# Performance work log

Hardware: AMD Instinct MI355X
Metric: run time of the kernel (lower is better)

## Reference

```python
import jax, jax.numpy as jnp
import numpy as np

THETA = 10000.0


def rope_apply(x, pos, theta=THETA):
    # x: [..., S, d] with d even; rotates interleaved pairs (2k, 2k+1),
    # matching the block-diag 2x2 rotation matmul in the torch RoPE.
    d = x.shape[-1]
    half = d // 2
    inv_freq = 1.0 / (theta ** (2.0 * jnp.arange(half, dtype=jnp.float32) / d))
    ang = pos.astype(jnp.float32)[:, None] * inv_freq[None, :]  # [S, half]
    cos, sin = jnp.cos(ang), jnp.sin(ang)
    xe, xo = x[..., 0::2], x[..., 1::2]
    oe = cos * xe - sin * xo
    oo = sin * xe + cos * xo
    return jnp.stack([oe, oo], axis=-1).reshape(x.shape)


def setup_inputs() -> dict:
    key = jax.random.key(0)
    ks = jax.random.split(key, 5)
    B, S, D = 2, 2048, 1024
    scale = 0.02
    return {
        "x": jax.random.normal(ks[0], (B, S, D), dtype=jnp.float32),
        "token_positions": jnp.arange(S, dtype=jnp.int64 if jax.config.jax_enable_x64 else jnp.int32),
        "wq": jax.random.normal(ks[1], (D, D), dtype=jnp.float32) * scale,
        "wk": jax.random.normal(ks[2], (D, D), dtype=jnp.float32) * scale,
        "wv": jax.random.normal(ks[3], (D, D), dtype=jnp.float32) * scale,
        "wo": jax.random.normal(ks[4], (D, D), dtype=jnp.float32) * scale,
    }


def reference(x, token_positions, wq, wk, wv, wo):
    B, S, D = x.shape
    H = 16
    dk = D // H

    def split_heads(t):  # [B,S,D] -> [B,H,S,dk]
        return t.reshape(B, S, H, dk).swapaxes(1, 2)

    q = split_heads(jnp.einsum('bsd,ed->bse', x, wq))
    k = split_heads(jnp.einsum('bsd,ed->bse', x, wk))
    v = split_heads(jnp.einsum('bsd,ed->bse', x, wv))

    q = rope_apply(q, token_positions)
    k = rope_apply(k, token_positions)

    scores = jnp.einsum('bhqd,bhkd->bhqk', q, k) / jnp.sqrt(jnp.float32(dk))
    causal = jnp.tril(jnp.ones((S, S), dtype=bool))
    scores = jnp.where(causal, scores, -jnp.inf)
    p = jax.nn.softmax(scores, axis=-1)
    o = jnp.einsum('bhqk,bhkd->bhqd', p, v)          # [B,H,S,dk]
    o = o.swapaxes(1, 2).reshape(B, S, D)            # merge heads
    return jnp.einsum('bse,de->bsd', o, wo)          # out proj (wo.T)
```

## Files before the change

kernel.cpp:

```cpp
#include <hip/hip_runtime.h>

typedef unsigned short u16;
typedef __attribute__((ext_vector_type(8))) short short8;
typedef __attribute__((ext_vector_type(4))) float f32x4;

__device__ __forceinline__ u16 f2b(float f) {
  union { float f; unsigned u; } v; v.f = f;
  unsigned u = v.u;
  return (u16)((u + 0x7FFFu + ((u >> 16) & 1u)) >> 16);
}
__device__ __forceinline__ u16 f2b_trunc(float f) {
  union { float f; unsigned u; } v; v.f = f;
  return (u16)(v.u >> 16);
}
__device__ __forceinline__ void glds16(const u16* g, u16* l) {
  __builtin_amdgcn_global_load_lds((const __attribute__((address_space(1))) void*)g,
                                   (__attribute__((address_space(3))) void*)l, 16, 0, 0);
}

__global__ __launch_bounds__(256) void prep_k(const float* __restrict__ x,
                                              const float* __restrict__ wq,
                                              const float* __restrict__ wk,
                                              const float* __restrict__ wv,
                                              const float* __restrict__ wo,
                                              const int* __restrict__ pos,
                                              u16* __restrict__ xb,
                                              u16* __restrict__ wqkvb,
                                              u16* __restrict__ wob,
                                              float* __restrict__ ct,
                                              float* __restrict__ st) {
  int bx = blockIdx.x, tid = threadIdx.x;
  if (bx < 8192) {
    const float* src; u16* dst; int base;
    if (bx < 4096)      { src = x;  dst = xb;                base = bx; }
    else if (bx < 5120) { src = wq; dst = wqkvb;             base = bx - 4096; }
    else if (bx < 6144) { src = wk; dst = wqkvb + (1 << 20); base = bx - 5120; }
    else if (bx < 7168) { src = wv; dst = wqkvb + (2 << 20); base = bx - 6144; }
    else                { src = wo; dst = wob;               base = bx - 7168; }
    int i4 = base * 1024 + tid * 4;
    const float4 v = *(const float4*)(src + i4);
    uint2 o;
    o.x = (unsigned)f2b(v.x) | ((unsigned)f2b(v.y) << 16);
    o.y = (unsigned)f2b(v.z) | ((unsigned)f2b(v.w) << 16);
    *(uint2*)(dst + i4) = o;
  } else {
    int idx = (bx - 8192) * 256 + tid;
    int i = idx & 31, s = idx >> 5;
    float p = (float)pos[s];
    float inv = expf(-(float)i * (logf(10000.0f) / 32.0f));
    float ang = p * inv;
    ct[idx] = cosf(ang);
    st[idx] = sinf(ang);
  }
}

__global__ __launch_bounds__(256) void gemm_qkv(const u16* __restrict__ A,
                                                const u16* __restrict__ B,
                                                const float* __restrict__ ct,
                                                const float* __restrict__ st,
                                                u16* __restrict__ Qr,
                                                u16* __restrict__ Kr,
                                                u16* __restrict__ VTg) {
  const int M = 4096, N = 3072, K = 1024;
  (void)M; (void)N;
  __shared__ u16 As[128 * 32];
  __shared__ u16 Bs[128 * 32];
  const int tid = threadIdx.x;
  const int wv = tid >> 6, lane = tid & 63;
  const int quad = lane >> 4, l16 = lane & 15;
  const int wm = wv & 1, wn = wv >> 1;
  const int m0 = blockIdx.y * 128, n0 = blockIdx.x * 128;

  f32x4 acc[4][4];
  for (int i = 0; i < 4; i++)
    for (int j = 0; j < 4; j++) acc[i][j] = (f32x4){0.f, 0.f, 0.f, 0.f};

  for (int kt = 0; kt < K; kt += 32) {
    __syncthreads();
#pragma unroll
    for (int pass = 0; pass < 2; pass++) {
      int c = pass * 256 + tid;
      int row = c >> 2, k8 = c & 3;
      glds16(A + (size_t)(m0 + row) * K + kt + k8 * 8, As + (size_t)(c & ~63) * 8);
      glds16(B + (size_t)(n0 + row) * K + kt + k8 * 8, Bs + (size_t)(c & ~63) * 8);
    }
    __syncthreads();
    short8 af[4], bfr[4];
#pragma unroll
    for (int i = 0; i < 4; i++)
      af[i] = *(const short8*)(As + (wm * 64 + i * 16 + l16) * 32 + quad * 8);
#pragma unroll
    for (int j = 0; j < 4; j++)
      bfr[j] = *(const short8*)(Bs + (wn * 64 + j * 16 + l16) * 32 + quad * 8);
#pragma unroll
    for (int i = 0; i < 4; i++)
#pragma unroll
      for (int j = 0; j < 4; j++)
        acc[i][j] = __builtin_amdgcn_mfma_f32_16x16x32_bf16(af[i], bfr[j], acc[i][j], 0, 0, 0);
  }

  const int region = n0 >> 10;
  if (region < 2) {
    u16* dst = region ? Kr : Qr;
    const int par = l16 & 1;
    for (int i = 0; i < 4; i++)
      for (int j = 0; j < 4; j++) {
        int col = n0 + wn * 64 + j * 16 + l16;
        int cq = col & 1023;
        int h = cq >> 6, d = cq & 63, ifr = (d >> 1) & 31;
        for (int r = 0; r < 4; r++) {
          int row = m0 + wm * 64 + i * 16 + quad * 4 + r;
          int b = row >> 11, s = row & 2047;
          float v = acc[i][j][r];
          float vp = __shfl_xor(v, 1);
          float c = ct[s * 32 + ifr], sn = st[s * 32 + ifr];
          float o = par ? (sn * vp + c * v) : (c * v - sn * vp);
          dst[((size_t)(b * 16 + h) * 2048 + s) * 64 + d] = f2b(o);
        }
      }
  } else {
    for (int i = 0; i < 4; i++)
      for (int j = 0; j < 4; j++) {
        int col = n0 + wn * 64 + j * 16 + l16;
        int cq = col & 1023;
        int h = cq >> 6, d = cq & 63;
        for (int r = 0; r < 4; r++) {
          int row = m0 + wm * 64 + i * 16 + quad * 4 + r;
          int b = row >> 11, s = row & 2047;
          VTg[((size_t)(b * 16 + h) * 64 + d) * 2048 + s] = f2b(acc[i][j][r]);
        }
      }
  }
}

__global__ __launch_bounds__(256) void gemm_bt_f32(const u16* __restrict__ A,
                                                   const u16* __restrict__ B,
                                                   float* __restrict__ C,
                                                   int M, int N, int K) {
  __shared__ u16 As[128 * 32];
  __shared__ u16 Bs[128 * 32];
  const int tid = threadIdx.x;
  const int wv = tid >> 6, lane = tid & 63;
  const int quad = lane >> 4, l16 = lane & 15;
  const int wm = wv & 1, wn = wv >> 1;
  const int m0 = blockIdx.y * 128, n0 = blockIdx.x * 128;

  f32x4 acc[4][4];
  for (int i = 0; i < 4; i++)
    for (int j = 0; j < 4; j++) acc[i][j] = (f32x4){0.f, 0.f, 0.f, 0.f};

  for (int kt = 0; kt < K; kt += 32) {
    __syncthreads();
#pragma unroll
    for (int pass = 0; pass < 2; pass++) {
      int c = pass * 256 + tid;
      int row = c >> 2, k8 = c & 3;
      glds16(A + (size_t)(m0 + row) * K + kt + k8 * 8, As + (size_t)(c & ~63) * 8);
      glds16(B + (size_t)(n0 + row) * K + kt + k8 * 8, Bs + (size_t)(c & ~63) * 8);
    }
    __syncthreads();
    short8 af[4], bfr[4];
#pragma unroll
    for (int i = 0; i < 4; i++)
      af[i] = *(const short8*)(As + (wm * 64 + i * 16 + l16) * 32 + quad * 8);
#pragma unroll
    for (int j = 0; j < 4; j++)
      bfr[j] = *(const short8*)(Bs + (wn * 64 + j * 16 + l16) * 32 + quad * 8);
#pragma unroll
    for (int i = 0; i < 4; i++)
#pragma unroll
      for (int j = 0; j < 4; j++)
        acc[i][j] = __builtin_amdgcn_mfma_f32_16x16x32_bf16(af[i], bfr[j], acc[i][j], 0, 0, 0);
  }
  for (int i = 0; i < 4; i++)
    for (int j = 0; j < 4; j++) {
      int col = n0 + wn * 64 + j * 16 + l16;
      for (int r = 0; r < 4; r++) {
        int row = m0 + wm * 64 + i * 16 + quad * 4 + r;
        C[(size_t)row * N + col] = acc[i][j][r];
      }
    }
}

__global__ __launch_bounds__(256) void attn_k(const u16* __restrict__ Q,
                                              const u16* __restrict__ K,
                                              const u16* __restrict__ VT,
                                              float* __restrict__ Op,
                                              float* __restrict__ Lp, int S) {
  __shared__ u16 Qs[8 * 512], Ks[8 * 512], Vt[64 * 64], Ps[8 * 520];
  const int tid = threadIdx.x;
  const int wv = tid >> 6, lane = tid & 63, quad = lane >> 4, l16 = lane & 15;
  const int bh = blockIdx.y, par = blockIdx.z;
  const u16* Qg = Q + (size_t)bh * S * 64;
  const u16* Kg = K + (size_t)bh * S * 64;
  const u16* Vg = VT + (size_t)bh * S * 64;
  const int nqt = S >> 6;
  const float scale2 = 0.125f * 1.44269504f;
  const int rowbase = wv * 16 + quad * 4;
  float* Opb = Op + ((size_t)par * 32 + bh) * S * 64;
  float* Lpb = Lp + ((size_t)par * 32 + bh) * S;

  const int vrow_off = lane >> 3;
  const int vchunk = (lane & 7) ^ (lane >> 3);

  for (int t = 0; t < 2; t++) {
    const int qt = t ? (nqt - 1 - (int)blockIdx.x) : (int)blockIdx.x;
    const int q0 = qt * 64;
    for (int p = wv; p < 8; p += 4)
      glds16(Qg + (size_t)(q0 + lane) * 64 + p * 8, Qs + p * 512);
    __syncthreads();
    short8 qa0 = *(const short8*)(Qs + quad * 512 + (wv * 16 + l16) * 8);
    short8 qa1 = *(const short8*)(Qs + (4 + quad) * 512 + (wv * 16 + l16) * 8);

    f32x4 oacc[4];
    for (int j = 0; j < 4; j++) oacc[j] = (f32x4){0.f, 0.f, 0.f, 0.f};
    float l_r[4] = {0.f, 0.f, 0.f, 0.f};

    for (int kt = par; kt <= qt; kt += 2) {
      const int k0 = kt * 64;
      __syncthreads();
      for (int p = wv; p < 8; p += 4) {
        glds16(Kg + (size_t)(k0 + lane) * 64 + p * 8, Ks + p * 512);
        glds16(Vg + (size_t)(p * 8 + vrow_off) * S + k0 + vchunk * 8, Vt + p * 512);
      }
      __syncthreads();

      const bool diag = (kt == qt);
#pragma unroll
      for (int nt = 0; nt < 4; nt++) {
        f32x4 s4 = (f32x4){0.f, 0.f, 0.f, 0.f};
        short8 b0 = *(const short8*)(Ks + quad * 512 + (nt * 16 + l16) * 8);
        short8 b1 = *(const short8*)(Ks + (4 + quad) * 512 + (nt * 16 + l16) * 8);
        s4 = __builtin_amdgcn_mfma_f32_16x16x32_bf16(qa0, b0, s4, 0, 0, 0);
        s4 = __builtin_amdgcn_mfma_f32_16x16x32_bf16(qa1, b1, s4, 0, 0, 0);
        int col = nt * 16 + l16;
        int cp = col >> 3, co = col & 7;
#pragma unroll
        for (int r = 0; r < 4; r++) {
          float v = s4[r] * scale2;
          v = fminf(v, 86.f);
          if (diag && col > rowbase + r) v = -1e30f;
          float p = exp2f(v);
          l_r[r] += p;
          int row = rowbase + r;
          int A = (cp + 2 * (row >> 3)) & 7;
          Ps[A * 520 + row * 8 + co] = f2b_trunc(p);
        }
      }
      {
        int mr = wv * 16 + l16;
        int A0 = (quad + 2 * (mr >> 3)) & 7;
        short8 pa0 = *(const short8*)(Ps + A0 * 520 + mr * 8);
        short8 pa1 = *(const short8*)(Ps + ((A0 + 4) & 7) * 520 + mr * 8);
        int sl0 = quad ^ (l16 & 7);
#pragma unroll
        for (int nt = 0; nt < 4; nt++) {
          int d = nt * 16 + l16;
          short8 vb0 = *(const short8*)(Vt + d * 64 + sl0 * 8);
          short8 vb1 = *(const short8*)(Vt + d * 64 + (sl0 ^ 4) * 8);
          oacc[nt] = __builtin_amdgcn_mfma_f32_16x16x32_bf16(pa0, vb0, oacc[nt], 0, 0, 0);
          oacc[nt] = __builtin_amdgcn_mfma_f32_16x16x32_bf16(pa1, vb1, oacc[nt], 0, 0, 0);
        }
      }
    }
#pragma unroll
    for (int r = 0; r < 4; r++) {
      l_r[r] += __shfl_xor(l_r[r], 1);
      l_r[r] += __shfl_xor(l_r[r], 2);
      l_r[r] += __shfl_xor(l_r[r], 4);
      l_r[r] += __shfl_xor(l_r[r], 8);
    }
    if (l16 == 0)
#pragma unroll
      for (int r = 0; r < 4; r++) Lpb[q0 + rowbase + r] = l_r[r];
#pragma unroll
    for (int nt = 0; nt < 4; nt++) {
      int col = nt * 16 + l16;
#pragma unroll
      for (int r = 0; r < 4; r++)
        Opb[(size_t)(q0 + rowbase + r) * 64 + col] = oacc[nt][r];
    }
    __syncthreads();
  }
}

__global__ __launch_bounds__(256) void combine_k(const float* __restrict__ Op,
                                                 const float* __restrict__ Lp,
                                                 u16* __restrict__ O, int S) {
  int idx = blockIdx.x * 256 + threadIdx.x;
  int d4 = idx & 15, s = (idx >> 4) & 2047, bh = idx >> 15;
  size_t po = (((size_t)bh * S) + s) * 64 + d4 * 4;
  size_t pstride = (size_t)32 * S * 64;
  float4 a = *(const float4*)(Op + po);
  float4 c = *(const float4*)(Op + pstride + po);
  float l = Lp[(size_t)bh * S + s] + Lp[(size_t)32 * S + (size_t)bh * S + s];
  float rl = 1.f / l;
  int b = bh >> 4, h = bh & 15;
  size_t oo = ((size_t)(b * S + s) * 16 + h) * 64 + d4 * 4;
  uint2 o;
  o.x = (unsigned)f2b((a.x + c.x) * rl) | ((unsigned)f2b((a.y + c.y) * rl) << 16);
  o.y = (unsigned)f2b((a.z + c.z) * rl) | ((unsigned)f2b((a.w + c.w) * rl) << 16);
  *(uint2*)(O + oo) = o;
}

extern "C" void kernel_launch(void* const* d_in, const int* in_sizes, int n_in,
                              void* d_out, int out_size, void* d_ws, size_t ws_size,
                              hipStream_t stream) {
  const float* x  = (const float*)d_in[0];
  const int*   tp = (const int*)d_in[1];
  const float* wq = (const float*)d_in[2];
  const float* wk = (const float*)d_in[3];
  const float* wvp = (const float*)d_in[4];
  const float* wo = (const float*)d_in[5];
  float* out = (float*)d_out;

  const int B = 2, S = 2048, D = 1024;
  const int BS = B * S;
  (void)B; (void)D;

  char* ws = (char*)d_ws;
  u16*   xb    = (u16*)(ws);
  u16*   wqkvb = (u16*)(ws + ((size_t)8 << 20));
  u16*   wob   = (u16*)(ws + ((size_t)14 << 20));
  float* ct    = (float*)(ws + ((size_t)16 << 20));
  float* st    = (float*)(ws + ((size_t)16 << 20) + (256 << 10));
  u16*   qr    = (u16*)(ws + ((size_t)17 << 20));
  u16*   kr    = (u16*)(ws + ((size_t)25 << 20));
  u16*   vtg   = (u16*)(ws + ((size_t)33 << 20));
  float* lpart = (float*)(ws + ((size_t)41 << 20));
  u16*   ob    = (u16*)(ws + ((size_t)42 << 20));
  float* opart = (float*)(ws + ((size_t)50 << 20));

  prep_k<<<8448, 256, 0, stream>>>(x, wq, wk, wvp, wo, tp, xb, wqkvb, wob, ct, st);

  dim3 g1(3 * D / 128, BS / 128);
  gemm_qkv<<<g1, 256, 0, stream>>>(xb, wqkvb, ct, st, qr, kr, vtg);

  dim3 ga(S / 128, 32, 2);
  attn_k<<<ga, 256, 0, stream>>>(qr, kr, vtg, opart, lpart, S);

  combine_k<<<(32 * S * 16) / 256, 256, 0, stream>>>(opart, lpart, ob, S);

  dim3 g2(D / 128, BS / 128);
  gemm_bt_f32<<<g2, 256, 0, stream>>>(ob, wob, out, BS, D, D);
}
```

Before: 216.2 us.

## Swizzle GEMM LDS tiles and vectorize QKV epilogue stores

```diff
diff --git a/kernel.cpp b/kernel.cpp
--- a/kernel.cpp
+++ b/kernel.cpp
@@ -27,8 +27,7 @@
                                               u16* __restrict__ xb,
                                               u16* __restrict__ wqkvb,
                                               u16* __restrict__ wob,
-                                              float* __restrict__ ct,
-                                              float* __restrict__ st) {
+                                              float* __restrict__ cs) {
   int bx = blockIdx.x, tid = threadIdx.x;
   if (bx < 8192) {
     const float* src; u16* dst; int base;
@@ -49,20 +48,18 @@
     float p = (float)pos[s];
     float inv = expf(-(float)i * (logf(10000.0f) / 32.0f));
     float ang = p * inv;
-    ct[idx] = cosf(ang);
-    st[idx] = sinf(ang);
+    cs[idx * 2]     = cosf(ang);
+    cs[idx * 2 + 1] = sinf(ang);
   }
 }
 
 __global__ __launch_bounds__(256) void gemm_qkv(const u16* __restrict__ A,
                                                 const u16* __restrict__ B,
-                                                const float* __restrict__ ct,
-                                                const float* __restrict__ st,
+                                                const float* __restrict__ cs,
                                                 u16* __restrict__ Qr,
                                                 u16* __restrict__ Kr,
                                                 u16* __restrict__ VTg) {
-  const int M = 4096, N = 3072, K = 1024;
-  (void)M; (void)N;
+  const int K = 1024;
   __shared__ u16 As[128 * 32];
   __shared__ u16 Bs[128 * 32];
   const int tid = threadIdx.x;
@@ -70,6 +67,7 @@
   const int quad = lane >> 4, l16 = lane & 15;
   const int wm = wv & 1, wn = wv >> 1;
   const int m0 = blockIdx.y * 128, n0 = blockIdx.x * 128;
+  const int kk = (quad ^ ((l16 >> 1) & 3)) * 8;
 
   f32x4 acc[4][4];
   for (int i = 0; i < 4; i++)
@@ -80,7 +78,7 @@
 #pragma unroll
     for (int pass = 0; pass < 2; pass++) {
       int c = pass * 256 + tid;
-      int row = c >> 2, k8 = c & 3;
+      int row = c >> 2, k8 = (c & 3) ^ ((row >> 1) & 3);
       glds16(A + (size_t)(m0 + row) * K + kt + k8 * 8, As + (size_t)(c & ~63) * 8);
       glds16(B + (size_t)(n0 + row) * K + kt + k8 * 8, Bs + (size_t)(c & ~63) * 8);
     }
@@ -88,10 +86,10 @@
     short8 af[4], bfr[4];
 #pragma unroll
     for (int i = 0; i < 4; i++)
-      af[i] = *(const short8*)(As + (wm * 64 + i * 16 + l16) * 32 + quad * 8);
+      af[i] = *(const short8*)(As + (wm * 64 + i * 16 + l16) * 32 + kk);
 #pragma unroll
     for (int j = 0; j < 4; j++)
-      bfr[j] = *(const short8*)(Bs + (wn * 64 + j * 16 + l16) * 32 + quad * 8);
+      bfr[j] = *(const short8*)(Bs + (wn * 64 + j * 16 + l16) * 32 + kk);
 #pragma unroll
     for (int i = 0; i < 4; i++)
 #pragma unroll
@@ -100,36 +98,42 @@
   }
 
   const int region = n0 >> 10;
+  const int b = m0 >> 11;
   if (region < 2) {
     u16* dst = region ? Kr : Qr;
-    const int par = l16 & 1;
+    const bool evn = (l16 & 1) == 0;
     for (int i = 0; i < 4; i++)
       for (int j = 0; j < 4; j++) {
         int col = n0 + wn * 64 + j * 16 + l16;
         int cq = col & 1023;
         int h = cq >> 6, d = cq & 63, ifr = (d >> 1) & 31;
         for (int r = 0; r < 4; r++) {
-          int row = m0 + wm * 64 + i * 16 + quad * 4 + r;
-          int b = row >> 11, s = row & 2047;
+          int s = (m0 & 2047) + wm * 64 + i * 16 + quad * 4 + r;
           float v = acc[i][j][r];
           float vp = __shfl_xor(v, 1);
-          float c = ct[s * 32 + ifr], sn = st[s * 32 + ifr];
-          float o = par ? (sn * vp + c * v) : (c * v - sn * vp);
-          dst[((size_t)(b * 16 + h) * 2048 + s) * 64 + d] = f2b(o);
+          if (evn) {
+            float2 c2 = *(const float2*)(cs + (s * 32 + ifr) * 2);
+            float oe = c2.x * v - c2.y * vp;
+            float oo = c2.y * v + c2.x * vp;
+            unsigned pk = (unsigned)f2b(oe) | ((unsigned)f2b(oo) << 16);
+            *(unsigned*)(dst + ((size_t)(b * 16 + h) * 2048 + s) * 64 + d) = pk;
+          }
         }
       }
   } else {
-    for (int i = 0; i < 4; i++)
-      for (int j = 0; j < 4; j++) {
-        int col = n0 + wn * 64 + j * 16 + l16;
-        int cq = col & 1023;
-        int h = cq >> 6, d = cq & 63;
-        for (int r = 0; r < 4; r++) {
-          int row = m0 + wm * 64 + i * 16 + quad * 4 + r;
-          int b = row >> 11, s = row & 2047;
-          VTg[((size_t)(b * 16 + h) * 64 + d) * 2048 + s] = f2b(acc[i][j][r]);
-        }
-      }
+    for (int j = 0; j < 4; j++) {
+      int col = n0 + wn * 64 + j * 16 + l16;
+      int cq = col & 1023;
+      int h = cq >> 6, d = cq & 63;
+      u16* base = VTg + ((size_t)(b * 16 + h) * 64 + d) * 2048;
+      for (int i = 0; i < 4; i++) {
+        int s0 = (m0 & 2047) + wm * 64 + i * 16 + quad * 4;
+        uint2 o;
+        o.x = (unsigned)f2b(acc[i][j][0]) | ((unsigned)f2b(acc[i][j][1]) << 16);
+        o.y = (unsigned)f2b(acc[i][j][2]) | ((unsigned)f2b(acc[i][j][3]) << 16);
+        *(uint2*)(base + s0) = o;
+      }
+    }
   }
 }
 
@@ -144,6 +148,7 @@
   const int quad = lane >> 4, l16 = lane & 15;
   const int wm = wv & 1, wn = wv >> 1;
   const int m0 = blockIdx.y * 128, n0 = blockIdx.x * 128;
+  const int kk = (quad ^ ((l16 >> 1) & 3)) * 8;
 
   f32x4 acc[4][4];
   for (int i = 0; i < 4; i++)
@@ -154,7 +159,7 @@
 #pragma unroll
     for (int pass = 0; pass < 2; pass++) {
       int c = pass * 256 + tid;
-      int row = c >> 2, k8 = c & 3;
+      int row = c >> 2, k8 = (c & 3) ^ ((row >> 1) & 3);
       glds16(A + (size_t)(m0 + row) * K + kt + k8 * 8, As + (size_t)(c & ~63) * 8);
       glds16(B + (size_t)(n0 + row) * K + kt + k8 * 8, Bs + (size_t)(c & ~63) * 8);
     }
@@ -162,10 +167,10 @@
     short8 af[4], bfr[4];
 #pragma unroll
     for (int i = 0; i < 4; i++)
-      af[i] = *(const short8*)(As + (wm * 64 + i * 16 + l16) * 32 + quad * 8);
+      af[i] = *(const short8*)(As + (wm * 64 + i * 16 + l16) * 32 + kk);
 #pragma unroll
     for (int j = 0; j < 4; j++)
-      bfr[j] = *(const short8*)(Bs + (wn * 64 + j * 16 + l16) * 32 + quad * 8);
+      bfr[j] = *(const short8*)(Bs + (wn * 64 + j * 16 + l16) * 32 + kk);
 #pragma unroll
     for (int i = 0; i < 4; i++)
 #pragma unroll
@@ -314,16 +319,14 @@
   const float* wo = (const float*)d_in[5];
   float* out = (float*)d_out;
 
-  const int B = 2, S = 2048, D = 1024;
-  const int BS = B * S;
-  (void)B; (void)D;
+  const int S = 2048, D = 1024;
+  const int BS = 2 * S;
 
   char* ws = (char*)d_ws;
   u16*   xb    = (u16*)(ws);
   u16*   wqkvb = (u16*)(ws + ((size_t)8 << 20));
   u16*   wob   = (u16*)(ws + ((size_t)14 << 20));
-  float* ct    = (float*)(ws + ((size_t)16 << 20));
-  float* st    = (float*)(ws + ((size_t)16 << 20) + (256 << 10));
+  float* cs    = (float*)(ws + ((size_t)16 << 20));
   u16*   qr    = (u16*)(ws + ((size_t)17 << 20));
   u16*   kr    = (u16*)(ws + ((size_t)25 << 20));
   u16*   vtg   = (u16*)(ws + ((size_t)33 << 20));
@@ -331,10 +334,10 @@
   u16*   ob    = (u16*)(ws + ((size_t)42 << 20));
   float* opart = (float*)(ws + ((size_t)50 << 20));
 
-  prep_k<<<8448, 256, 0, stream>>>(x, wq, wk, wvp, wo, tp, xb, wqkvb, wob, ct, st);
+  prep_k<<<8448, 256, 0, stream>>>(x, wq, wk, wvp, wo, tp, xb, wqkvb, wob, cs);
 
   dim3 g1(3 * D / 128, BS / 128);
-  gemm_qkv<<<g1, 256, 0, stream>>>(xb, wqkvb, ct, st, qr, kr, vtg);
+  gemm_qkv<<<g1, 256, 0, stream>>>(xb, wqkvb, cs, qr, kr, vtg);
 
   dim3 ga(S / 128, 32, 2);
   attn_k<<<ga, 256, 0, stream>>>(qr, kr, vtg, opart, lpart, S);
```

New measurement: 235.5 us. +8.9%, slower.
